# Kernel tuning notes

Hardware: AMD Instinct MI355X
Metric: run time of the kernel (lower is better)

Reference implementation:

```python
import jax, jax.numpy as jnp
import numpy as np

B, S, IN_DIM, OUT_DIM = 8, 8192, 1024, 1024


def setup_inputs() -> dict:
    key = jax.random.key(0)
    k1, k2, k3, k4 = jax.random.split(key, 4)
    x = jax.random.normal(k1, (B, S, IN_DIM), dtype=jnp.float32)
    visual_mask = jax.random.randint(k2, (B, S), 0, 2) == 1  # bool [B,S]
    # nn.Linear weights are [out_dim, in_dim]
    w_v = jax.random.normal(k3, (OUT_DIM, IN_DIM), dtype=jnp.float32) * (IN_DIM ** -0.5)
    w_t = jax.random.normal(k4, (OUT_DIM, IN_DIM), dtype=jnp.float32) * (IN_DIM ** -0.5)
    return {"x": x, "visual_mask": visual_mask, "w_v": w_v, "w_t": w_t}


def reference(x, visual_mask, w_v, w_t):
    # Per-token routed dual linear: out[b,s] = x[b,s] @ (w_v if mask else w_t).T
    out_v = jnp.einsum("bsi,oi->bso", x, w_v)  # [B,S,OUT]
    out_t = jnp.einsum("bsi,oi->bso", x, w_t)  # [B,S,OUT]
    return jnp.where(visual_mask[:, :, None], out_v, out_t)
```

## Files before the change

### kernel.cpp

```cpp
#include <hip/hip_runtime.h>
#include <stdint.h>

#define TOKENS 65536
#define KDIM 1024
#define NDIM 1024
#define MROWS 65664
#define ROWTILES 513

using short8 = __attribute__((ext_vector_type(8))) short;
using f32x4  = __attribute__((ext_vector_type(4))) float;

#define ASYNC_COPY16(g, l) __builtin_amdgcn_global_load_lds( \
    (const __attribute__((address_space(1))) void*)(g),      \
    (__attribute__((address_space(3))) void*)(l), 16, 0, 0)

__device__ __forceinline__ short f2bf(float f) {
    union { float f; unsigned u; } c; c.f = f;
    unsigned r = c.u + 0x7FFFu + ((c.u >> 16) & 1u);
    return (short)(r >> 16);
}

__global__ __launch_bounds__(256) void detect_mask_fmt(const unsigned* __restrict__ mask,
                                                       int* __restrict__ hdr) {
    int mode = 0;
    for (int i = threadIdx.x; i < 16384; i += 256) {
        unsigned w = mask[i];
        if (w == 0x3F800000u) { mode = 2; break; }
        if (w > 1u) mode = 1;
    }
    if (mode) atomicMax(&hdr[2], mode);
}

__device__ __forceinline__ bool read_mask(const void* mask, int fmt, int t) {
    if (fmt == 2) return ((const float*)mask)[t] != 0.0f;
    if (fmt == 1) return ((const unsigned char*)mask)[t] != 0;
    return ((const int*)mask)[t] != 0;
}

__global__ __launch_bounds__(256) void route_assign(const void* __restrict__ mask,
                                                    int* __restrict__ rowmap,
                                                    int* __restrict__ slotmap,
                                                    int* __restrict__ hdr) {
    const int tid  = threadIdx.x;
    const int lane = tid & 63;
    const int wid  = tid >> 6;
    const int t    = blockIdx.x * 256 + tid;
    const int fmt  = hdr[2];
    const bool m   = read_mask(mask, fmt, t);

    unsigned long long bal = __ballot(m);
    int vpre = __popcll(bal & ((1ull << lane) - 1ull));
    int vcnt = __popcll(bal);
    int tpre = lane - vpre;
    int tcnt = 64 - vcnt;

    __shared__ int cv[4], ct[4], ov[4], ot[4];
    __shared__ int bv, bt;
    if (lane == 0) { cv[wid] = vcnt; ct[wid] = tcnt; }
    __syncthreads();
    if (tid == 0) {
        int sv = 0, st = 0;
        for (int w = 0; w < 4; ++w) { ov[w] = sv; sv += cv[w]; ot[w] = st; st += ct[w]; }
        bv = atomicAdd(&hdr[0], sv);
        bt = atomicAdd(&hdr[1], st);
    }
    __syncthreads();
    int slot = m ? (bv + ov[wid] + vpre)
                 : (MROWS - 1 - (bt + ot[wid] + tpre));
    rowmap[slot] = t;
    slotmap[t] = slot;
}

__global__ __launch_bounds__(256) void gather_convert(const float* __restrict__ x,
                                                      const int* __restrict__ slotmap,
                                                      short* __restrict__ Abuf) {
    const int lane = threadIdx.x & 63;
    const int t    = blockIdx.x * 4 + (threadIdx.x >> 6);
    const int slot = slotmap[t];
    const float* src = x + (size_t)t * KDIM;
    short* dst = Abuf + (size_t)slot * KDIM;
#pragma unroll
    for (int p = 0; p < 4; ++p) {
        int k = p * 256 + lane * 4;
        float4 v = *(const float4*)(src + k);
        short4 o;
        o.x = f2bf(v.x); o.y = f2bf(v.y); o.z = f2bf(v.z); o.w = f2bf(v.w);
        *(short4*)(dst + k) = o;
    }
}

__global__ __launch_bounds__(256) void convert_weights(const float* __restrict__ wv,
                                                       const float* __restrict__ wt,
                                                       short* __restrict__ ovp,
                                                       short* __restrict__ otp) {
    int i = (blockIdx.x * 256 + threadIdx.x) * 4;
    const float* src; short* dst; int off;
    if (i < NDIM * KDIM) { src = wv; dst = ovp; off = i; }
    else                 { src = wt; dst = otp; off = i - NDIM * KDIM; }
    float4 v = *(const float4*)(src + off);
    short4 o;
    o.x = f2bf(v.x); o.y = f2bf(v.y); o.z = f2bf(v.z); o.w = f2bf(v.w);
    *(short4*)(dst + off) = o;
}

__global__ __launch_bounds__(256) void gemm_routed(const short* __restrict__ Abuf,
                                                   const short* __restrict__ Wv,
                                                   const short* __restrict__ Wt,
                                                   const int* __restrict__ rowmap,
                                                   const int* __restrict__ hdr,
                                                   float* __restrict__ out) {
    __shared__ __align__(16) short As[128 * 32];
    __shared__ __align__(16) short Bs[128 * 32];
    __shared__ int rmap_s[128];

    const int Mv = hdr[0];
    const int r0 = blockIdx.y * 128;
    if (r0 == Mv) return;
    const int n0 = blockIdx.x * 128;
    const short* Wsel = (r0 < Mv) ? Wv : Wt;

    const int tid  = threadIdx.x;
    const int lane = tid & 63;
    const int wvid = tid >> 6;

    if (tid < 128) rmap_s[tid] = rowmap[r0 + tid];

    const int srow = wvid * 16 + (lane >> 2);
    const int koct = (lane & 3) * 8;
    const short* aP = Abuf + (size_t)(r0 + srow) * KDIM + koct;
    const short* bP = Wsel + (size_t)(n0 + srow) * KDIM + koct;
    char* lA = (char*)As + wvid * 1024;
    char* lB = (char*)Bs + wvid * 1024;

    f32x4 acc[4][4];
#pragma unroll
    for (int i = 0; i < 4; ++i)
#pragma unroll
        for (int j = 0; j < 4; ++j) acc[i][j] = f32x4{0.f, 0.f, 0.f, 0.f};

    const int wm = (wvid & 1) * 64;
    const int wn = (wvid >> 1) * 64;
    const short* aF = As + (wm + (lane & 15)) * 32 + (lane >> 4) * 8;
    const short* bF = Bs + (wn + (lane & 15)) * 32 + (lane >> 4) * 8;

    for (int kt = 0; kt < KDIM / 32; ++kt) {
        const int k0 = kt * 32;
        __syncthreads();
        ASYNC_COPY16(aP + k0,             lA);
        ASYNC_COPY16(aP + 64 * KDIM + k0, lA + 4096);
        ASYNC_COPY16(bP + k0,             lB);
        ASYNC_COPY16(bP + 64 * KDIM + k0, lB + 4096);
        __syncthreads();

        short8 af[4], bf[4];
#pragma unroll
        for (int mt = 0; mt < 4; ++mt) af[mt] = *(const short8*)(aF + mt * 16 * 32);
#pragma unroll
        for (int nt = 0; nt < 4; ++nt) bf[nt] = *(const short8*)(bF + nt * 16 * 32);
#pragma unroll
        for (int mt = 0; mt < 4; ++mt)
#pragma unroll
            for (int nt = 0; nt < 4; ++nt)
                acc[mt][nt] = __builtin_amdgcn_mfma_f32_16x16x32_bf16(
                    af[mt], bf[nt], acc[mt][nt], 0, 0, 0);
    }

    const int col = n0 + wn + (lane & 15);
#pragma unroll
    for (int mt = 0; mt < 4; ++mt) {
        int rb = wm + mt * 16 + ((lane >> 4) << 2);
#pragma unroll
        for (int i = 0; i < 4; ++i) {
            int token = rmap_s[rb + i];
            if (token < 0) continue;
            float* orow = out + (size_t)token * NDIM + col;
            orow[0]  = acc[mt][0][i];
            orow[16] = acc[mt][1][i];
            orow[32] = acc[mt][2][i];
            orow[48] = acc[mt][3][i];
        }
    }
}

__global__ __launch_bounds__(256) void fallback_matvec(const float* __restrict__ x,
                                                       const void* __restrict__ mask,
                                                       const float* __restrict__ wv,
                                                       const float* __restrict__ wt,
                                                       const int* __restrict__ hdr,
                                                       float* __restrict__ out) {
    __shared__ float xs[KDIM];
    const int t = blockIdx.x;
    const int fmt = hdr[2];
    const bool m = read_mask(mask, fmt, t);
    const float* w = m ? wv : wt;
    const float* src = x + (size_t)t * KDIM;
    for (int k = threadIdx.x; k < KDIM; k += 256) xs[k] = src[k];
    __syncthreads();
    for (int n = threadIdx.x; n < NDIM; n += 256) {
        const float* wr = w + (size_t)n * KDIM;
        float s = 0.f;
        for (int k = 0; k < KDIM; ++k) s += xs[k] * wr[k];
        out[(size_t)t * NDIM + n] = s;
    }
}

extern "C" void kernel_launch(void* const* d_in, const int* in_sizes, int n_in,
                              void* d_out, int out_size, void* d_ws, size_t ws_size,
                              hipStream_t stream) {
    const float* x    = (const float*)d_in[0];
    const void*  mask = d_in[1];
    const float* w_v  = (const float*)d_in[2];
    const float* w_t  = (const float*)d_in[3];
    float* out = (float*)d_out;

    char* ws = (char*)d_ws;
    int*   hdr     = (int*)ws;
    int*   rowmap  = (int*)(ws + 4096);
    int*   slotmap = (int*)(ws + 270336);
    short* wvb     = (short*)(ws + 532480);
    short* wtb     = (short*)(ws + 2629632);
    short* Abuf    = (short*)(ws + 4726784);
    const size_t need = 4726784ull + (size_t)MROWS * KDIM * sizeof(short);

    if (ws_size >= need) {
        hipMemsetAsync(hdr, 0, 4096, stream);
        hipMemsetAsync(rowmap, 0xFF, MROWS * sizeof(int), stream);
        detect_mask_fmt<<<1, 256, 0, stream>>>((const unsigned*)mask, hdr);
        route_assign<<<TOKENS / 256, 256, 0, stream>>>(mask, rowmap, slotmap, hdr);
        gather_convert<<<TOKENS / 4, 256, 0, stream>>>(x, slotmap, Abuf);
        convert_weights<<<(2 * NDIM * KDIM) / (256 * 4), 256, 0, stream>>>(w_v, w_t, wvb, wtb);
        gemm_routed<<<dim3(8, ROWTILES), 256, 0, stream>>>(Abuf, wvb, wtb, rowmap, hdr, out);
    } else {
        hipMemsetAsync(hdr, 0, 16, stream);
        detect_mask_fmt<<<1, 256, 0, stream>>>((const unsigned*)mask, hdr);
        fallback_matvec<<<TOKENS, 256, 0, stream>>>(x, mask, w_v, w_t, hdr, out);
    }
}
```

Baseline: 748.1 us.

## Double GEMM K-tile to 64, remap blocks for XCD locality, parallelize mask detection

Raises the GEMM K-step from 32 to 64, so each sync pair covers two MFMA k-substeps and the number of barriers per tile is halved. The 1D grid is remapped so consecutive block ids are spread across row tiles in a pattern meant to keep blocks that share data on the same XCD/L2. The single-block mask-format detection loop becomes a 64-block one-element-per-thread kernel. This doubles LDS per block, which may lower occupancy, and bank conflicts may change with the new 128-byte row stride.

```diff
diff --git a/kernel.cpp b/kernel.cpp
--- a/kernel.cpp
+++ b/kernel.cpp
@@ -6,6 +6,7 @@
 #define NDIM 1024
 #define MROWS 65664
 #define ROWTILES 513
+#define BK 64
 
 using short8 = __attribute__((ext_vector_type(8))) short;
 using f32x4  = __attribute__((ext_vector_type(4))) float;
@@ -22,12 +23,11 @@
 
 __global__ __launch_bounds__(256) void detect_mask_fmt(const unsigned* __restrict__ mask,
                                                        int* __restrict__ hdr) {
+    int i = blockIdx.x * 256 + threadIdx.x;
+    unsigned w = mask[i];
     int mode = 0;
-    for (int i = threadIdx.x; i < 16384; i += 256) {
-        unsigned w = mask[i];
-        if (w == 0x3F800000u) { mode = 2; break; }
-        if (w > 1u) mode = 1;
-    }
+    if (w == 0x3F800000u)      mode = 2;
+    else if (w > 1u)           mode = 1;
     if (mode) atomicMax(&hdr[2], mode);
 }
 
@@ -109,14 +109,17 @@
                                                    const int* __restrict__ rowmap,
                                                    const int* __restrict__ hdr,
                                                    float* __restrict__ out) {
-    __shared__ __align__(16) short As[128 * 32];
-    __shared__ __align__(16) short Bs[128 * 32];
+    __shared__ __align__(16) short As[128 * BK];
+    __shared__ __align__(16) short Bs[128 * BK];
     __shared__ int rmap_s[128];
 
+    const int bid = blockIdx.x;
+    const int w   = (bid & 7) * ROWTILES + (bid >> 3);
+    const int r0  = (w >> 3) * 128;
+    const int n0  = (w & 7) * 128;
+
     const int Mv = hdr[0];
-    const int r0 = blockIdx.y * 128;
     if (r0 == Mv) return;
-    const int n0 = blockIdx.x * 128;
     const short* Wsel = (r0 < Mv) ? Wv : Wt;
 
     const int tid  = threadIdx.x;
@@ -125,12 +128,12 @@
 
     if (tid < 128) rmap_s[tid] = rowmap[r0 + tid];
 
-    const int srow = wvid * 16 + (lane >> 2);
-    const int koct = (lane & 3) * 8;
-    const short* aP = Abuf + (size_t)(r0 + srow) * KDIM + koct;
-    const short* bP = Wsel + (size_t)(n0 + srow) * KDIM + koct;
-    char* lA = (char*)As + wvid * 1024;
-    char* lB = (char*)Bs + wvid * 1024;
+    const int srow = wvid * 32 + (lane >> 3);
+    const int scol = (lane & 7) * 8;
+    const short* aP = Abuf + (size_t)(r0 + srow) * KDIM + scol;
+    const short* bP = Wsel + (size_t)(n0 + srow) * KDIM + scol;
+    char* lA = (char*)As + wvid * 4096;
+    char* lB = (char*)Bs + wvid * 4096;
 
     f32x4 acc[4][4];
 #pragma unroll
@@ -140,29 +143,33 @@
 
     const int wm = (wvid & 1) * 64;
     const int wn = (wvid >> 1) * 64;
-    const short* aF = As + (wm + (lane & 15)) * 32 + (lane >> 4) * 8;
-    const short* bF = Bs + (wn + (lane & 15)) * 32 + (lane >> 4) * 8;
-
-    for (int kt = 0; kt < KDIM / 32; ++kt) {
-        const int k0 = kt * 32;
+    const short* aF = As + (wm + (lane & 15)) * BK + (lane >> 4) * 8;
+    const short* bF = Bs + (wn + (lane & 15)) * BK + (lane >> 4) * 8;
+
+    for (int kt = 0; kt < KDIM / BK; ++kt) {
+        const int k0 = kt * BK;
         __syncthreads();
-        ASYNC_COPY16(aP + k0,             lA);
-        ASYNC_COPY16(aP + 64 * KDIM + k0, lA + 4096);
-        ASYNC_COPY16(bP + k0,             lB);
-        ASYNC_COPY16(bP + 64 * KDIM + k0, lB + 4096);
+#pragma unroll
+        for (int c = 0; c < 4; ++c) {
+            ASYNC_COPY16(aP + (size_t)c * 8 * KDIM + k0, lA + c * 1024);
+            ASYNC_COPY16(bP + (size_t)c * 8 * KDIM + k0, lB + c * 1024);
+        }
         __syncthreads();
 
-        short8 af[4], bf[4];
-#pragma unroll
-        for (int mt = 0; mt < 4; ++mt) af[mt] = *(const short8*)(aF + mt * 16 * 32);
-#pragma unroll
-        for (int nt = 0; nt < 4; ++nt) bf[nt] = *(const short8*)(bF + nt * 16 * 32);
-#pragma unroll
-        for (int mt = 0; mt < 4; ++mt)
-#pragma unroll
-            for (int nt = 0; nt < 4; ++nt)
-                acc[mt][nt] = __builtin_amdgcn_mfma_f32_16x16x32_bf16(
-                    af[mt], bf[nt], acc[mt][nt], 0, 0, 0);
+#pragma unroll
+        for (int ks = 0; ks < 2; ++ks) {
+            short8 af[4], bfr[4];
+#pragma unroll
+            for (int mt = 0; mt < 4; ++mt) af[mt]  = *(const short8*)(aF + mt * 16 * BK + ks * 32);
+#pragma unroll
+            for (int nt = 0; nt < 4; ++nt) bfr[nt] = *(const short8*)(bF + nt * 16 * BK + ks * 32);
+#pragma unroll
+            for (int mt = 0; mt < 4; ++mt)
+#pragma unroll
+                for (int nt = 0; nt < 4; ++nt)
+                    acc[mt][nt] = __builtin_amdgcn_mfma_f32_16x16x32_bf16(
+                        af[mt], bfr[nt], acc[mt][nt], 0, 0, 0);
+        }
     }
 
     const int col = n0 + wn + (lane & 15);
@@ -223,16 +230,16 @@
     const size_t need = 4726784ull + (size_t)MROWS * KDIM * sizeof(short);
 
     if (ws_size >= need) {
-        hipMemsetAsync(hdr, 0, 4096, stream);
+        hipMemsetAsync(hdr, 0, 16, stream);
         hipMemsetAsync(rowmap, 0xFF, MROWS * sizeof(int), stream);
-        detect_mask_fmt<<<1, 256, 0, stream>>>((const unsigned*)mask, hdr);
+        detect_mask_fmt<<<64, 256, 0, stream>>>((const unsigned*)mask, hdr);
         route_assign<<<TOKENS / 256, 256, 0, stream>>>(mask, rowmap, slotmap, hdr);
         gather_convert<<<TOKENS / 4, 256, 0, stream>>>(x, slotmap, Abuf);
         convert_weights<<<(2 * NDIM * KDIM) / (256 * 4), 256, 0, stream>>>(w_v, w_t, wvb, wtb);
-        gemm_routed<<<dim3(8, ROWTILES), 256, 0, stream>>>(Abuf, wvb, wtb, rowmap, hdr, out);
+        gemm_routed<<<8 * ROWTILES, 256, 0, stream>>>(Abuf, wvb, wtb, rowmap, hdr, out);
     } else {
         hipMemsetAsync(hdr, 0, 16, stream);
-        detect_mask_fmt<<<1, 256, 0, stream>>>((const unsigned*)mask, hdr);
+        detect_mask_fmt<<<64, 256, 0, stream>>>((const unsigned*)mask, hdr);
         fallback_matvec<<<TOKENS, 256, 0, stream>>>(x, mask, w_v, w_t, hdr, out);
     }
 }
```

Result: faster. 709.5 us (-5.2%).
